# Kernel tuning notes

Hardware: AMD Instinct MI355X
Metric: run time of the kernel (lower is better)

The kernel has to match this reference:

```python
import jax, jax.numpy as jnp
import numpy as np
from jax import lax

T = 32768
DUNITS = 1024
ATT_DIM = 512
EPROJS = 512
ACONV_CHANS = 32
ACONV_FILTS = 15  # kernel = 2*15+1 = 31


def setup_inputs() -> dict:
    key = jax.random.key(0)
    ks = jax.random.split(key, 8)
    dec_z = jax.random.normal(ks[0], (1, DUNITS), jnp.float32)
    att_prev = jax.random.uniform(ks[1], (1, T), jnp.float32)
    att_prev = att_prev / jnp.sum(att_prev, axis=1, keepdims=True)  # prob-like alignment
    pre_compute_enc_h = jax.random.normal(ks[2], (1, T, ATT_DIM), jnp.float32) * 0.1
    enc_h = jax.random.normal(ks[3], (1, T, EPROJS), jnp.float32)
    mask = jnp.zeros((1, T), jnp.float32)  # additive mask (0 = keep)
    conv_w = jax.random.normal(ks[4], (ACONV_CHANS, 1, 2 * ACONV_FILTS + 1), jnp.float32) * 0.1
    conv_b = jnp.zeros((ACONV_CHANS,), jnp.float32)
    W_att = jax.random.normal(ks[5], (ATT_DIM, ACONV_CHANS), jnp.float32) * 0.1
    W_dec = jax.random.normal(ks[6], (ATT_DIM, DUNITS), jnp.float32) * 0.03
    W_g = jax.random.normal(ks[7], (1, ATT_DIM), jnp.float32) * 0.05
    b_g = jnp.zeros((1,), jnp.float32)
    return {"dec_z": dec_z, "att_prev": att_prev, "pre_compute_enc_h": pre_compute_enc_h,
            "enc_h": enc_h, "mask": mask, "conv_w": conv_w, "conv_b": conv_b,
            "W_att": W_att, "W_dec": W_dec, "W_g": W_g, "b_g": b_g}


def reference(dec_z, att_prev, pre_compute_enc_h, enc_h, mask, conv_w, conv_b, W_att, W_dec, W_g, b_g):
    scaling = 2.0
    # location conv: att_prev [1,T] -> [1,C,T] (Conv2d with height-1 kernel == Conv1d)
    att_conv = lax.conv_general_dilated(
        att_prev[:, None, :], conv_w, window_strides=(1,),
        padding=[(ACONV_FILTS, ACONV_FILTS)],
        dimension_numbers=("NCH", "OIH", "NCH"))
    att_conv = att_conv + conv_b[None, :, None]          # [1,C,T]
    att_conv = jnp.einsum("bct,ac->bta", att_conv, W_att)  # mlp_att -> [1,T,att_dim]
    dec_z_tiled = (dec_z @ W_dec.T)[:, None, :]           # [1,1,att_dim]
    # gvec over tanh sum -> energies [1,T]
    e = jnp.einsum("bta,a->bt", jnp.tanh(pre_compute_enc_h + dec_z_tiled + att_conv), W_g[0]) + b_g[0]
    e = e + mask
    w = jax.nn.softmax(scaling * e, axis=1)               # [1,T]
    # forward-attention recurrence: shift-add-mul, then L1 normalize
    att_prev_shift = jnp.pad(att_prev, ((0, 0), (1, 0)))[:, :-1]
    w = (att_prev + att_prev_shift) * w
    w = jnp.clip(w, 1e-6, None)
    w = w / jnp.sum(w, axis=1, keepdims=True)             # L1 normalize (w > 0)
    c = jnp.sum(enc_h * w[:, :, None], axis=1)            # [1,eprojs]
    return (c, w)
```

## Files before the change

kernel.cpp:

```cpp
#include <hip/hip_runtime.h>

#define T_LEN 32768
#define ADIM  512
#define NDEC  1024
#define KTAPS 31

#define WS_BASE 0
#define WS_G    512
#define WS_CREP 0
#define WS_SARR 16384
#define WS_BMAX 49152
#define WS_BSUM 49664
#define WS_SSUM 50178
#define WS_U    50432

__device__ __forceinline__ float fast_tanh(float x) {
    float e = __expf(2.0f * x);
    return 1.0f - 2.0f * __builtin_amdgcn_rcpf(e + 1.0f);
}

__device__ __forceinline__ float uniform_f(float v) {
    return __uint_as_float(__builtin_amdgcn_readfirstlane(__float_as_uint(v)));
}

__global__ __launch_bounds__(256) void k0_prep(
        const float* __restrict__ dec_z, const float* __restrict__ conv_w,
        const float* __restrict__ conv_b, const float* __restrict__ W_att,
        const float* __restrict__ W_dec, float* __restrict__ ws) {
    int b = blockIdx.x, tid = threadIdx.x;
    int lane = tid & 63, wave = tid >> 6;
    if (b < 64) {
        for (int s = 0; s < 2; ++s) {
            int a = b * 8 + wave * 2 + s;
            float sum = 0.f;
            #pragma unroll
            for (int i = 0; i < 16; ++i)
                sum += W_dec[a * NDEC + i * 64 + lane] * dec_z[i * 64 + lane];
            #pragma unroll
            for (int off = 32; off > 0; off >>= 1) sum += __shfl_xor(sum, off);
            if (lane == 0) {
                float bias = 0.f;
                #pragma unroll
                for (int c = 0; c < 32; ++c) bias += conv_b[c] * W_att[a * 32 + c];
                ws[WS_BASE + a] = sum + bias;
            }
        }
    } else if (b < 64 + KTAPS) {
        int k = b - 64;
        for (int r = 0; r < 2; ++r) {
            int a = tid + r * 256;
            float g = 0.f;
            #pragma unroll
            for (int c = 0; c < 32; ++c) g += conv_w[c * KTAPS + k] * W_att[a * 32 + c];
            ws[WS_G + k * ADIM + a] = g;
        }
    } else {
        if (tid == 0) ws[WS_SSUM] = 0.f;
    }
}

__global__ __launch_bounds__(512, 4) void k1_energy(
        const float* __restrict__ att_prev, const float* __restrict__ pre,
        const float* __restrict__ mask, const float* __restrict__ W_g,
        const float* __restrict__ b_g, float* __restrict__ ws) {
    __shared__ float Gs[KTAPS * ADIM];
    __shared__ float ap_s[96];
    __shared__ float wm[8], wz[8];
    int tid = threadIdx.x, lane = tid & 63, wave = tid >> 6;
    int t0 = blockIdx.x * 64;

    const float4* Gsrc = (const float4*)(ws + WS_G);
    float4* Gdst = (float4*)Gs;
    #pragma unroll
    for (int i = 0; i < 8; ++i) {
        int idx = tid + i * 512;
        if (idx < 3968) Gdst[idx] = Gsrc[idx];
    }
    if (tid < 94) {
        int g = t0 - 15 + tid;
        ap_s[tid] = (g >= 0 && g < T_LEN) ? att_prev[g] : 0.f;
    }
    __syncthreads();

    float bg = b_g[0];
    int tb_local = wave * 8;
    int tb = t0 + tb_local;

    float ap_u[38];
    #pragma unroll
    for (int i = 0; i < 38; ++i) ap_u[i] = uniform_f(ap_s[tb_local + i]);

    float ps[8];
    #pragma unroll
    for (int j = 0; j < 8; ++j) ps[j] = 0.f;

    #pragma unroll 1
    for (int half = 0; half < 2; ++half) {
        int aa = half * 256 + 4 * lane;
        float4 base = *(const float4*)(ws + WS_BASE + aa);
        float4 wg   = *(const float4*)(W_g + aa);

        float4 p[8];
        #pragma unroll
        for (int j = 0; j < 8; ++j)
            p[j] = *(const float4*)(pre + (size_t)(tb + j) * ADIM + aa);

        float4 acc[8];
        #pragma unroll
        for (int j = 0; j < 8; ++j) acc[j] = base;

        #pragma unroll
        for (int k = 0; k < KTAPS; ++k) {
            float4 g = *(const float4*)(&Gs[k * ADIM + aa]);
            #pragma unroll
            for (int j = 0; j < 8; ++j) {
                float apv = ap_u[j + k];
                acc[j].x = fmaf(apv, g.x, acc[j].x);
                acc[j].y = fmaf(apv, g.y, acc[j].y);
                acc[j].z = fmaf(apv, g.z, acc[j].z);
                acc[j].w = fmaf(apv, g.w, acc[j].w);
            }
        }
        #pragma unroll
        for (int j = 0; j < 8; ++j) {
            float s = ps[j];
            s = fmaf(fast_tanh(p[j].x + acc[j].x), wg.x, s);
            s = fmaf(fast_tanh(p[j].y + acc[j].y), wg.y, s);
            s = fmaf(fast_tanh(p[j].z + acc[j].z), wg.z, s);
            s = fmaf(fast_tanh(p[j].w + acc[j].w), wg.w, s);
            ps[j] = s;
        }
    }

    float m_run = -1e30f, z_run = 0.f;
    #pragma unroll
    for (int j = 0; j < 8; ++j) {
        float e = ps[j];
        #pragma unroll
        for (int off = 32; off > 0; off >>= 1) e += __shfl_xor(e, off);
        int t = tb + j;
        float sv = 2.0f * (e + bg + mask[t]);
        float mn = fmaxf(m_run, sv);
        z_run = z_run * __expf(m_run - mn) + __expf(sv - mn);
        m_run = mn;
        if (lane == 0) ws[WS_SARR + t] = sv;
    }
    if (lane == 0) { wm[wave] = m_run; wz[wave] = z_run; }
    __syncthreads();
    if (tid == 0) {
        float M = wm[0], Z = wz[0];
        #pragma unroll
        for (int w = 1; w < 8; ++w) {
            float mn = fmaxf(M, wm[w]);
            Z = Z * __expf(M - mn) + wz[w] * __expf(wm[w] - mn);
            M = mn;
        }
        ws[WS_BMAX + blockIdx.x] = M;
        ws[WS_BSUM + blockIdx.x] = Z;
    }
}

__global__ __launch_bounds__(256) void k2_weights(
        const float* __restrict__ att_prev, float* __restrict__ ws) {
    __shared__ float sm[256], sz[256];
    __shared__ float wsum[4];
    int tid = threadIdx.x;
    if (tid < 128) ws[WS_CREP + blockIdx.x * 128 + tid] = 0.f;

    float m1 = ws[WS_BMAX + tid],       z1 = ws[WS_BSUM + tid];
    float m2 = ws[WS_BMAX + tid + 256], z2 = ws[WS_BSUM + tid + 256];
    float M = fmaxf(m1, m2);
    float Z = z1 * __expf(m1 - M) + z2 * __expf(m2 - M);
    sm[tid] = M; sz[tid] = Z;
    __syncthreads();
    for (int s = 128; s > 0; s >>= 1) {
        if (tid < s) {
            float ma = sm[tid], mb = sm[tid + s];
            float mn = fmaxf(ma, mb);
            sz[tid] = sz[tid] * __expf(ma - mn) + sz[tid + s] * __expf(mb - mn);
            sm[tid] = mn;
        }
        __syncthreads();
    }
    M = sm[0];
    float invZ = 1.0f / sz[0];
    int t = blockIdx.x * 256 + tid;
    float pair = att_prev[t] + ((t > 0) ? att_prev[t - 1] : 0.f);
    float u = fmaxf(pair * __expf(ws[WS_SARR + t] - M) * invZ, 1e-6f);
    ws[WS_U + t] = u;
    float s = u;
    #pragma unroll
    for (int off = 32; off > 0; off >>= 1) s += __shfl_xor(s, off);
    int lane = tid & 63, wave = tid >> 6;
    if (lane == 0) wsum[wave] = s;
    __syncthreads();
    if (tid == 0) atomicAdd(&ws[WS_SSUM], wsum[0] + wsum[1] + wsum[2] + wsum[3]);
}

__global__ __launch_bounds__(512) void k3_context(
        const float* __restrict__ enc_h, float* __restrict__ ws,
        float* __restrict__ out) {
    __shared__ float cbuf[4 * 512];
    int tid = threadIdx.x;
    int team = tid >> 7, l = tid & 127;
    int a4 = 4 * l;
    int t0 = blockIdx.x * 32;
    float invS = 1.0f / ws[WS_SSUM];
    if (tid < 32) out[512 + t0 + tid] = ws[WS_U + t0 + tid] * invS;
    int tbase = t0 + team * 8;
    float4 acc = make_float4(0.f, 0.f, 0.f, 0.f);
    #pragma unroll
    for (int i = 0; i < 8; ++i) {
        int t = tbase + i;
        float wt = ws[WS_U + t] * invS;
        float4 e = *(const float4*)(enc_h + (size_t)t * ADIM + a4);
        acc.x = fmaf(wt, e.x, acc.x);
        acc.y = fmaf(wt, e.y, acc.y);
        acc.z = fmaf(wt, e.z, acc.z);
        acc.w = fmaf(wt, e.w, acc.w);
    }
    if (team != 0) *(float4*)&cbuf[team * 512 + a4] = acc;
    __syncthreads();
    if (team == 0) {
        float4 b1 = *(const float4*)&cbuf[1 * 512 + a4];
        float4 b2 = *(const float4*)&cbuf[2 * 512 + a4];
        float4 b3 = *(const float4*)&cbuf[3 * 512 + a4];
        float* rep = ws + WS_CREP + (blockIdx.x & 31) * 512;
        atomicAdd(&rep[a4 + 0], acc.x + b1.x + b2.x + b3.x);
        atomicAdd(&rep[a4 + 1], acc.y + b1.y + b2.y + b3.y);
        atomicAdd(&rep[a4 + 2], acc.z + b1.z + b2.z + b3.z);
        atomicAdd(&rep[a4 + 3], acc.w + b1.w + b2.w + b3.w);
    }
}

__global__ __launch_bounds__(256) void k4_final(
        const float* __restrict__ ws, float* __restrict__ out) {
    int a = blockIdx.x * 256 + threadIdx.x;
    float acc = 0.f;
    #pragma unroll
    for (int r = 0; r < 32; ++r) acc += ws[WS_CREP + r * 512 + a];
    out[a] = acc;
}

extern "C" void kernel_launch(void* const* d_in, const int* in_sizes, int n_in,
                              void* d_out, int out_size, void* d_ws, size_t ws_size,
                              hipStream_t stream) {
    const float* dec_z    = (const float*)d_in[0];
    const float* att_prev = (const float*)d_in[1];
    const float* pre      = (const float*)d_in[2];
    const float* enc_h    = (const float*)d_in[3];
    const float* mask     = (const float*)d_in[4];
    const float* conv_w   = (const float*)d_in[5];
    const float* conv_b   = (const float*)d_in[6];
    const float* W_att    = (const float*)d_in[7];
    const float* W_dec    = (const float*)d_in[8];
    const float* W_g      = (const float*)d_in[9];
    const float* b_g      = (const float*)d_in[10];
    float* out = (float*)d_out;
    float* ws  = (float*)d_ws;

    k0_prep   <<<96,   256, 0, stream>>>(dec_z, conv_w, conv_b, W_att, W_dec, ws);
    k1_energy <<<512,  512, 0, stream>>>(att_prev, pre, mask, W_g, b_g, ws);
    k2_weights<<<128,  256, 0, stream>>>(att_prev, ws);
    k3_context<<<1024, 512, 0, stream>>>(enc_h, ws, out);
    k4_final  <<<2,    256, 0, stream>>>(ws, out);
}
```

Measured before the change: 190.3 us.

## Split energy kernel over attention-dim halves with atomic partial sums, fuse final reduce

The energy kernel now assigns each block one half of the attention dimension over 32 timesteps. Partial tanh dot products are accumulated with atomicAdd into a zeroed score array, and the shared-memory G tile is halved. The intent is more blocks with a smaller LDS footprint for higher occupancy. The softmax statistics move into a new small kernel, and the final context reduction is folded into the context kernel through a last-block counter, removing one launch. The cost is an extra launch, atomics on the score array, and more zeroing work in the prep kernel.

Result: slower. 432.6 us (+127.3%).

```diff
diff --git a/kernel.cpp b/kernel.cpp
--- a/kernel.cpp
+++ b/kernel.cpp
@@ -10,8 +10,9 @@
 #define WS_CREP 0
 #define WS_SARR 16384
 #define WS_BMAX 49152
-#define WS_BSUM 49664
-#define WS_SSUM 50178
+#define WS_BSUM 49216
+#define WS_SSUM 49280
+#define WS_CTR  49284
 #define WS_U    50432
 
 __device__ __forceinline__ float fast_tanh(float x) {
@@ -54,35 +55,40 @@
             for (int c = 0; c < 32; ++c) g += conv_w[c * KTAPS + k] * W_att[a * 32 + c];
             ws[WS_G + k * ADIM + a] = g;
         }
+    } else if (b == 95) {
+        if (tid == 0) {
+            ws[WS_SSUM] = 0.f;
+            ((unsigned int*)ws)[WS_CTR] = 0u;
+        }
     } else {
-        if (tid == 0) ws[WS_SSUM] = 0.f;
-    }
-}
-
-__global__ __launch_bounds__(512, 4) void k1_energy(
+        int idx = (b - 96) * 1024 + tid * 4;
+        *(float4*)(ws + WS_SARR + idx) = make_float4(0.f, 0.f, 0.f, 0.f);
+    }
+}
+
+__global__ __launch_bounds__(256, 5) void k1_energy(
         const float* __restrict__ att_prev, const float* __restrict__ pre,
-        const float* __restrict__ mask, const float* __restrict__ W_g,
-        const float* __restrict__ b_g, float* __restrict__ ws) {
-    __shared__ float Gs[KTAPS * ADIM];
-    __shared__ float ap_s[96];
-    __shared__ float wm[8], wz[8];
+        const float* __restrict__ W_g, float* __restrict__ ws) {
+    __shared__ float Gs[KTAPS * 256];
+    __shared__ float ap_s[62];
     int tid = threadIdx.x, lane = tid & 63, wave = tid >> 6;
-    int t0 = blockIdx.x * 64;
-
-    const float4* Gsrc = (const float4*)(ws + WS_G);
-    float4* Gdst = (float4*)Gs;
+    int half = blockIdx.x & 1;
+    int t0 = (blockIdx.x >> 1) * 32;
+
     #pragma unroll
     for (int i = 0; i < 8; ++i) {
-        int idx = tid + i * 512;
-        if (idx < 3968) Gdst[idx] = Gsrc[idx];
-    }
-    if (tid < 94) {
+        int idx = tid + i * 256;
+        if (idx < 1984) {
+            int k = idx >> 6, col = idx & 63;
+            ((float4*)Gs)[idx] = *(const float4*)(ws + WS_G + k * ADIM + half * 256 + col * 4);
+        }
+    }
+    if (tid < 62) {
         int g = t0 - 15 + tid;
         ap_s[tid] = (g >= 0 && g < T_LEN) ? att_prev[g] : 0.f;
     }
     __syncthreads();
 
-    float bg = b_g[0];
     int tb_local = wave * 8;
     int tb = t0 + tb_local;
 
@@ -90,100 +96,94 @@
     #pragma unroll
     for (int i = 0; i < 38; ++i) ap_u[i] = uniform_f(ap_s[tb_local + i]);
 
-    float ps[8];
-    #pragma unroll
-    for (int j = 0; j < 8; ++j) ps[j] = 0.f;
-
-    #pragma unroll 1
-    for (int half = 0; half < 2; ++half) {
-        int aa = half * 256 + 4 * lane;
-        float4 base = *(const float4*)(ws + WS_BASE + aa);
-        float4 wg   = *(const float4*)(W_g + aa);
-
-        float4 p[8];
-        #pragma unroll
-        for (int j = 0; j < 8; ++j)
-            p[j] = *(const float4*)(pre + (size_t)(tb + j) * ADIM + aa);
-
-        float4 acc[8];
-        #pragma unroll
-        for (int j = 0; j < 8; ++j) acc[j] = base;
-
-        #pragma unroll
-        for (int k = 0; k < KTAPS; ++k) {
-            float4 g = *(const float4*)(&Gs[k * ADIM + aa]);
-            #pragma unroll
-            for (int j = 0; j < 8; ++j) {
-                float apv = ap_u[j + k];
-                acc[j].x = fmaf(apv, g.x, acc[j].x);
-                acc[j].y = fmaf(apv, g.y, acc[j].y);
-                acc[j].z = fmaf(apv, g.z, acc[j].z);
-                acc[j].w = fmaf(apv, g.w, acc[j].w);
-            }
-        }
+    int aa = 4 * lane;
+    float4 base = *(const float4*)(ws + WS_BASE + half * 256 + aa);
+    float4 wg   = *(const float4*)(W_g + half * 256 + aa);
+
+    float4 p[8];
+    #pragma unroll
+    for (int j = 0; j < 8; ++j)
+        p[j] = *(const float4*)(pre + (size_t)(tb + j) * ADIM + half * 256 + aa);
+
+    float4 acc[8];
+    #pragma unroll
+    for (int j = 0; j < 8; ++j) acc[j] = base;
+
+    #pragma unroll
+    for (int k = 0; k < KTAPS; ++k) {
+        float4 g = *(const float4*)(&Gs[k * 256 + aa]);
         #pragma unroll
         for (int j = 0; j < 8; ++j) {
-            float s = ps[j];
-            s = fmaf(fast_tanh(p[j].x + acc[j].x), wg.x, s);
-            s = fmaf(fast_tanh(p[j].y + acc[j].y), wg.y, s);
-            s = fmaf(fast_tanh(p[j].z + acc[j].z), wg.z, s);
-            s = fmaf(fast_tanh(p[j].w + acc[j].w), wg.w, s);
-            ps[j] = s;
-        }
-    }
-
-    float m_run = -1e30f, z_run = 0.f;
+            float apv = ap_u[j + k];
+            acc[j].x = fmaf(apv, g.x, acc[j].x);
+            acc[j].y = fmaf(apv, g.y, acc[j].y);
+            acc[j].z = fmaf(apv, g.z, acc[j].z);
+            acc[j].w = fmaf(apv, g.w, acc[j].w);
+        }
+    }
     #pragma unroll
     for (int j = 0; j < 8; ++j) {
-        float e = ps[j];
-        #pragma unroll
-        for (int off = 32; off > 0; off >>= 1) e += __shfl_xor(e, off);
-        int t = tb + j;
-        float sv = 2.0f * (e + bg + mask[t]);
-        float mn = fmaxf(m_run, sv);
-        z_run = z_run * __expf(m_run - mn) + __expf(sv - mn);
-        m_run = mn;
-        if (lane == 0) ws[WS_SARR + t] = sv;
-    }
-    if (lane == 0) { wm[wave] = m_run; wz[wave] = z_run; }
+        float s;
+        s = fast_tanh(p[j].x + acc[j].x) * wg.x;
+        s = fmaf(fast_tanh(p[j].y + acc[j].y), wg.y, s);
+        s = fmaf(fast_tanh(p[j].z + acc[j].z), wg.z, s);
+        s = fmaf(fast_tanh(p[j].w + acc[j].w), wg.w, s);
+        #pragma unroll
+        for (int off = 32; off > 0; off >>= 1) s += __shfl_xor(s, off);
+        if (lane == 0) atomicAdd(&ws[WS_SARR + tb + j], s);
+    }
+}
+
+__global__ __launch_bounds__(256) void k2a_stats(
+        const float* __restrict__ mask, const float* __restrict__ b_g,
+        float* __restrict__ ws) {
+    __shared__ float wm[4], wz[4];
+    int tid = threadIdx.x, lane = tid & 63, wave = tid >> 6;
+    ws[WS_CREP + blockIdx.x * 256 + tid] = 0.f;
+
+    float bg = b_g[0];
+    int t = blockIdx.x * 512 + tid;
+    float sv0 = 2.0f * (ws[WS_SARR + t] + bg + mask[t]);
+    float sv1 = 2.0f * (ws[WS_SARR + t + 256] + bg + mask[t + 256]);
+    ws[WS_SARR + t] = sv0;
+    ws[WS_SARR + t + 256] = sv1;
+    float M = fmaxf(sv0, sv1);
+    float Z = __expf(sv0 - M) + __expf(sv1 - M);
+    #pragma unroll
+    for (int off = 32; off > 0; off >>= 1) {
+        float Mo = __shfl_xor(M, off), Zo = __shfl_xor(Z, off);
+        float mn = fmaxf(M, Mo);
+        Z = Z * __expf(M - mn) + Zo * __expf(Mo - mn);
+        M = mn;
+    }
+    if (lane == 0) { wm[wave] = M; wz[wave] = Z; }
     __syncthreads();
     if (tid == 0) {
-        float M = wm[0], Z = wz[0];
-        #pragma unroll
-        for (int w = 1; w < 8; ++w) {
-            float mn = fmaxf(M, wm[w]);
-            Z = Z * __expf(M - mn) + wz[w] * __expf(wm[w] - mn);
-            M = mn;
-        }
-        ws[WS_BMAX + blockIdx.x] = M;
-        ws[WS_BSUM + blockIdx.x] = Z;
-    }
-}
-
-__global__ __launch_bounds__(256) void k2_weights(
+        float Mg = wm[0], Zg = wz[0];
+        #pragma unroll
+        for (int w = 1; w < 4; ++w) {
+            float mn = fmaxf(Mg, wm[w]);
+            Zg = Zg * __expf(Mg - mn) + wz[w] * __expf(wm[w] - mn);
+            Mg = mn;
+        }
+        ws[WS_BMAX + blockIdx.x] = Mg;
+        ws[WS_BSUM + blockIdx.x] = Zg;
+    }
+}
+
+__global__ __launch_bounds__(256) void k2b_weights(
         const float* __restrict__ att_prev, float* __restrict__ ws) {
-    __shared__ float sm[256], sz[256];
     __shared__ float wsum[4];
-    int tid = threadIdx.x;
-    if (tid < 128) ws[WS_CREP + blockIdx.x * 128 + tid] = 0.f;
-
-    float m1 = ws[WS_BMAX + tid],       z1 = ws[WS_BSUM + tid];
-    float m2 = ws[WS_BMAX + tid + 256], z2 = ws[WS_BSUM + tid + 256];
-    float M = fmaxf(m1, m2);
-    float Z = z1 * __expf(m1 - M) + z2 * __expf(m2 - M);
-    sm[tid] = M; sz[tid] = Z;
-    __syncthreads();
-    for (int s = 128; s > 0; s >>= 1) {
-        if (tid < s) {
-            float ma = sm[tid], mb = sm[tid + s];
-            float mn = fmaxf(ma, mb);
-            sz[tid] = sz[tid] * __expf(ma - mn) + sz[tid + s] * __expf(mb - mn);
-            sm[tid] = mn;
-        }
-        __syncthreads();
-    }
-    M = sm[0];
-    float invZ = 1.0f / sz[0];
+    int tid = threadIdx.x, lane = tid & 63, wave = tid >> 6;
+    float M = ws[WS_BMAX + lane], Z = ws[WS_BSUM + lane];
+    #pragma unroll
+    for (int off = 32; off > 0; off >>= 1) {
+        float Mo = __shfl_xor(M, off), Zo = __shfl_xor(Z, off);
+        float mn = fmaxf(M, Mo);
+        Z = Z * __expf(M - mn) + Zo * __expf(Mo - mn);
+        M = mn;
+    }
+    float invZ = 1.0f / Z;
     int t = blockIdx.x * 256 + tid;
     float pair = att_prev[t] + ((t > 0) ? att_prev[t - 1] : 0.f);
     float u = fmaxf(pair * __expf(ws[WS_SARR + t] - M) * invZ, 1e-6f);
@@ -191,7 +191,6 @@
     float s = u;
     #pragma unroll
     for (int off = 32; off > 0; off >>= 1) s += __shfl_xor(s, off);
-    int lane = tid & 63, wave = tid >> 6;
     if (lane == 0) wsum[wave] = s;
     __syncthreads();
     if (tid == 0) atomicAdd(&ws[WS_SSUM], wsum[0] + wsum[1] + wsum[2] + wsum[3]);
@@ -201,6 +200,7 @@
         const float* __restrict__ enc_h, float* __restrict__ ws,
         float* __restrict__ out) {
     __shared__ float cbuf[4 * 512];
+    __shared__ int is_last;
     int tid = threadIdx.x;
     int team = tid >> 7, l = tid & 127;
     int a4 = 4 * l;
@@ -230,16 +230,21 @@
         atomicAdd(&rep[a4 + 1], acc.y + b1.y + b2.y + b3.y);
         atomicAdd(&rep[a4 + 2], acc.z + b1.z + b2.z + b3.z);
         atomicAdd(&rep[a4 + 3], acc.w + b1.w + b2.w + b3.w);
-    }
-}
-
-__global__ __launch_bounds__(256) void k4_final(
-        const float* __restrict__ ws, float* __restrict__ out) {
-    int a = blockIdx.x * 256 + threadIdx.x;
-    float acc = 0.f;
-    #pragma unroll
-    for (int r = 0; r < 32; ++r) acc += ws[WS_CREP + r * 512 + a];
-    out[a] = acc;
+        __threadfence();
+    }
+    __syncthreads();
+    if (tid == 0) {
+        unsigned int old = atomicAdd(&((unsigned int*)ws)[WS_CTR], 1u);
+        is_last = (old == gridDim.x - 1);
+    }
+    __syncthreads();
+    if (is_last) {
+        __threadfence();
+        float accf = 0.f;
+        #pragma unroll
+        for (int r = 0; r < 32; ++r) accf += ws[WS_CREP + r * 512 + tid];
+        out[tid] = accf;
+    }
 }
 
 extern "C" void kernel_launch(void* const* d_in, const int* in_sizes, int n_in,
@@ -259,9 +264,9 @@
     float* out = (float*)d_out;
     float* ws  = (float*)d_ws;
 
-    k0_prep   <<<96,   256, 0, stream>>>(dec_z, conv_w, conv_b, W_att, W_dec, ws);
-    k1_energy <<<512,  512, 0, stream>>>(att_prev, pre, mask, W_g, b_g, ws);
-    k2_weights<<<128,  256, 0, stream>>>(att_prev, ws);
-    k3_context<<<1024, 512, 0, stream>>>(enc_h, ws, out);
-    k4_final  <<<2,    256, 0, stream>>>(ws, out);
-}
+    k0_prep    <<<128,  256, 0, stream>>>(dec_z, conv_w, conv_b, W_att, W_dec, ws);
+    k1_energy  <<<2048, 256, 0, stream>>>(att_prev, pre, W_g, ws);
+    k2a_stats  <<<64,   256, 0, stream>>>(mask, b_g, ws);
+    k2b_weights<<<128,  256, 0, stream>>>(att_prev, ws);
+    k3_context <<<1024, 512, 0, stream>>>(enc_h, ws, out);
+}
```

## Fuse softmax-weight kernel into context kernel and defer L1 normalization to final pass

Applied to the files above, without the earlier changes.

Removes the separate weights kernel. Each context block now redundantly reduces the 512 per-block softmax max/sum pairs, recomputes the unnormalized weights inline, and accumulates the weighted enc_h sums. The L1 normalization scale is applied once in the final kernel, which also writes the normalized weight output. The context-replica zeroing moves into the energy kernel and gets its own workspace region. This trades one kernel launch and a global round trip for a redundant per-block reduction and extra att_prev loads.

After: 189.9 us. About the same (-0.2%).

```diff
diff --git a/kernel.cpp b/kernel.cpp
--- a/kernel.cpp
+++ b/kernel.cpp
@@ -7,12 +7,12 @@
 
 #define WS_BASE 0
 #define WS_G    512
-#define WS_CREP 0
 #define WS_SARR 16384
 #define WS_BMAX 49152
 #define WS_BSUM 49664
-#define WS_SSUM 50178
+#define WS_SSUM 50176
 #define WS_U    50432
+#define WS_CREP 83968
 
 __device__ __forceinline__ float fast_tanh(float x) {
     float e = __expf(2.0f * x);
@@ -69,6 +69,8 @@
     int tid = threadIdx.x, lane = tid & 63, wave = tid >> 6;
     int t0 = blockIdx.x * 64;
 
+    if (blockIdx.x < 32) ws[WS_CREP + blockIdx.x * 512 + tid] = 0.f;
+
     const float4* Gsrc = (const float4*)(ws + WS_G);
     float4* Gdst = (float4*)Gs;
     #pragma unroll
@@ -160,66 +162,63 @@
     }
 }
 
-__global__ __launch_bounds__(256) void k2_weights(
-        const float* __restrict__ att_prev, float* __restrict__ ws) {
-    __shared__ float sm[256], sz[256];
-    __shared__ float wsum[4];
-    int tid = threadIdx.x;
-    if (tid < 128) ws[WS_CREP + blockIdx.x * 128 + tid] = 0.f;
-
-    float m1 = ws[WS_BMAX + tid],       z1 = ws[WS_BSUM + tid];
-    float m2 = ws[WS_BMAX + tid + 256], z2 = ws[WS_BSUM + tid + 256];
-    float M = fmaxf(m1, m2);
-    float Z = z1 * __expf(m1 - M) + z2 * __expf(m2 - M);
-    sm[tid] = M; sz[tid] = Z;
-    __syncthreads();
-    for (int s = 128; s > 0; s >>= 1) {
-        if (tid < s) {
-            float ma = sm[tid], mb = sm[tid + s];
-            float mn = fmaxf(ma, mb);
-            sz[tid] = sz[tid] * __expf(ma - mn) + sz[tid + s] * __expf(mb - mn);
-            sm[tid] = mn;
-        }
-        __syncthreads();
-    }
-    M = sm[0];
-    float invZ = 1.0f / sz[0];
-    int t = blockIdx.x * 256 + tid;
-    float pair = att_prev[t] + ((t > 0) ? att_prev[t - 1] : 0.f);
-    float u = fmaxf(pair * __expf(ws[WS_SARR + t] - M) * invZ, 1e-6f);
-    ws[WS_U + t] = u;
-    float s = u;
-    #pragma unroll
-    for (int off = 32; off > 0; off >>= 1) s += __shfl_xor(s, off);
-    int lane = tid & 63, wave = tid >> 6;
-    if (lane == 0) wsum[wave] = s;
-    __syncthreads();
-    if (tid == 0) atomicAdd(&ws[WS_SSUM], wsum[0] + wsum[1] + wsum[2] + wsum[3]);
-}
-
 __global__ __launch_bounds__(512) void k3_context(
-        const float* __restrict__ enc_h, float* __restrict__ ws,
-        float* __restrict__ out) {
+        const float* __restrict__ att_prev, const float* __restrict__ enc_h,
+        float* __restrict__ ws) {
+    __shared__ float wmz[16];
     __shared__ float cbuf[4 * 512];
-    int tid = threadIdx.x;
+    int tid = threadIdx.x, lane = tid & 63, wave = tid >> 6;
+
+    float m = ws[WS_BMAX + wave * 64 + lane];
+    float z = ws[WS_BSUM + wave * 64 + lane];
+    #pragma unroll
+    for (int off = 32; off > 0; off >>= 1) {
+        float mo = __shfl_xor(m, off), zo = __shfl_xor(z, off);
+        float mn = fmaxf(m, mo);
+        z = z * __expf(m - mn) + zo * __expf(mo - mn);
+        m = mn;
+    }
+    if (lane == 0) { wmz[wave] = m; wmz[8 + wave] = z; }
+    __syncthreads();
+    float M = wmz[0], Z = wmz[8];
+    #pragma unroll
+    for (int w = 1; w < 8; ++w) {
+        float mn = fmaxf(M, wmz[w]);
+        Z = Z * __expf(M - mn) + wmz[8 + w] * __expf(wmz[w] - mn);
+        M = mn;
+    }
+    float invZ = 1.0f / Z;
+
+    int t0 = blockIdx.x * 32;
     int team = tid >> 7, l = tid & 127;
     int a4 = 4 * l;
-    int t0 = blockIdx.x * 32;
-    float invS = 1.0f / ws[WS_SSUM];
-    if (tid < 32) out[512 + t0 + tid] = ws[WS_U + t0 + tid] * invS;
     int tbase = t0 + team * 8;
     float4 acc = make_float4(0.f, 0.f, 0.f, 0.f);
     #pragma unroll
     for (int i = 0; i < 8; ++i) {
         int t = tbase + i;
-        float wt = ws[WS_U + t] * invS;
+        float ap0 = att_prev[t];
+        float apm = (t > 0) ? att_prev[t - 1] : 0.f;
+        float u = fmaxf((ap0 + apm) * __expf(ws[WS_SARR + t] - M) * invZ, 1e-6f);
         float4 e = *(const float4*)(enc_h + (size_t)t * ADIM + a4);
-        acc.x = fmaf(wt, e.x, acc.x);
-        acc.y = fmaf(wt, e.y, acc.y);
-        acc.z = fmaf(wt, e.z, acc.z);
-        acc.w = fmaf(wt, e.w, acc.w);
+        acc.x = fmaf(u, e.x, acc.x);
+        acc.y = fmaf(u, e.y, acc.y);
+        acc.z = fmaf(u, e.z, acc.z);
+        acc.w = fmaf(u, e.w, acc.w);
     }
     if (team != 0) *(float4*)&cbuf[team * 512 + a4] = acc;
+
+    if (tid < 32) {
+        int t = t0 + tid;
+        float ap0 = att_prev[t];
+        float apm = (t > 0) ? att_prev[t - 1] : 0.f;
+        float u = fmaxf((ap0 + apm) * __expf(ws[WS_SARR + t] - M) * invZ, 1e-6f);
+        ws[WS_U + t] = u;
+        float s = u;
+        #pragma unroll
+        for (int off = 16; off > 0; off >>= 1) s += __shfl_xor(s, off, 32);
+        if (tid == 0) atomicAdd(&ws[WS_SSUM], s);
+    }
     __syncthreads();
     if (team == 0) {
         float4 b1 = *(const float4*)&cbuf[1 * 512 + a4];
@@ -233,13 +232,19 @@
     }
 }
 
-__global__ __launch_bounds__(256) void k4_final(
+__global__ __launch_bounds__(512) void k4_final(
         const float* __restrict__ ws, float* __restrict__ out) {
-    int a = blockIdx.x * 256 + threadIdx.x;
-    float acc = 0.f;
-    #pragma unroll
-    for (int r = 0; r < 32; ++r) acc += ws[WS_CREP + r * 512 + a];
-    out[a] = acc;
+    int b = blockIdx.x, tid = threadIdx.x;
+    float invS = 1.0f / ws[WS_SSUM];
+    if (b == 0) {
+        float acc = 0.f;
+        #pragma unroll
+        for (int r = 0; r < 32; ++r) acc += ws[WS_CREP + r * 512 + tid];
+        out[tid] = acc * invS;
+    } else {
+        int i = (b - 1) * 512 + tid;
+        out[512 + i] = ws[WS_U + i] * invS;
+    }
 }
 
 extern "C" void kernel_launch(void* const* d_in, const int* in_sizes, int n_in,
@@ -261,7 +266,6 @@
 
     k0_prep   <<<96,   256, 0, stream>>>(dec_z, conv_w, conv_b, W_att, W_dec, ws);
     k1_energy <<<512,  512, 0, stream>>>(att_prev, pre, mask, W_g, b_g, ws);
-    k2_weights<<<128,  256, 0, stream>>>(att_prev, ws);
-    k3_context<<<1024, 512, 0, stream>>>(enc_h, ws, out);
-    k4_final  <<<2,    256, 0, stream>>>(ws, out);
-}
+    k3_context<<<1024, 512, 0, stream>>>(att_prev, enc_h, ws);
+    k4_final  <<<65,   512, 0, stream>>>(ws, out);
+}
```
